# Kernel tuning notes

Measured on AMD Instinct MI355X. Metric: run time of the kernel, lower is better.

The kernel has to match this reference:

```python
import jax, jax.numpy as jnp
import numpy as np

S, B, D, A = 8192, 64, 512, 256


def setup_inputs() -> dict:
    key = jax.random.key(0)
    ks = jax.random.split(key, 7)
    return {
        "x": jax.random.normal(ks[0], (S, B, D), dtype=jnp.float32),
        "h": jax.random.normal(ks[1], (1, B, D), dtype=jnp.float32),
        "Wx": jax.random.normal(ks[2], (A, D), dtype=jnp.float32) * (1.0 / np.sqrt(D)),
        "bx": jax.random.normal(ks[3], (A,), dtype=jnp.float32) * 0.01,
        "Wh": jax.random.normal(ks[4], (A, D), dtype=jnp.float32) * (1.0 / np.sqrt(D)),
        "Wt": jax.random.normal(ks[5], (1, A), dtype=jnp.float32) * (1.0 / np.sqrt(A)),
        "bt": jax.random.normal(ks[6], (1,), dtype=jnp.float32) * 0.01,
    }


def reference(x, h, Wx, bx, Wh, Wt, bt):
    # x: (S, B, D) seq-first; h: (1, B, D) hidden state.
    # All Conv1d ops have kernel size 1 -> plain per-position matmuls.
    xb = jnp.transpose(x, (1, 0, 2))               # (B, S, D)
    wx = jnp.einsum('bsd,ad->bas', xb, Wx) + bx[None, :, None]   # (B, A, S)
    h0 = h.transpose(1, 0, 2).reshape(-1, h.shape[-1])           # (B, D)
    wh = h0 @ Wh.T                                                # (B, A)
    # score conv (A -> 1) on tanh(wx + wh), then softmax over seq dim
    score = jnp.einsum('a,bas->bs', Wt[0], jnp.tanh(wx + wh[:, :, None])) + bt[0]  # (B, S)
    attn = jax.nn.softmax(score, axis=-1)                         # (B, S)
    out = jnp.einsum('bs,bsd->bd', attn, xb)                      # (B, D)
    return out
```

## Files before the change

### kernel.cpp

```cpp
#include <hip/hip_runtime.h>


#define S_DIM 8192
#define B_DIM 64
#define D_DIM 512
#define A_DIM 256
#define BM 32
#define NTILES 256

typedef _Float16 half8 __attribute__((ext_vector_type(8)));
typedef float f32x4 __attribute__((ext_vector_type(4)));

__device__ __forceinline__ float tanh_fast(float x) {
  float e = __expf(2.0f * x);
  return 1.0f - 2.0f * __builtin_amdgcn_rcpf(e + 1.0f);
}

__global__ void __launch_bounds__(256)
convw_kernel(const float* __restrict__ Wx, _Float16* __restrict__ Wp) {
  const int idx = (blockIdx.x * 256 + threadIdx.x) * 8;
  const int a = idx >> 9;
  const int k = idx & 511;
  f32x4 va = *(const f32x4*)(Wx + idx);
  f32x4 vb = *(const f32x4*)(Wx + idx + 4);
  half8 hx;
#pragma unroll
  for (int i = 0; i < 4; ++i) { hx[i] = (_Float16)va[i]; hx[4 + i] = (_Float16)vb[i]; }
  const int ta = a >> 4, fr = a & 15;
  const int tk = k >> 5, fg = (k >> 3) & 3;
  *(half8*)(Wp + (ta * 16 + tk) * 512 + (fg * 16 + fr) * 8) = hx;
}

__global__ void __launch_bounds__(256)
whb_kernel(const float* __restrict__ h, const float* __restrict__ Wh,
           const float* __restrict__ bx, float* __restrict__ whb) {
  __shared__ float hs[D_DIM];
  const int b = blockIdx.x, tid = threadIdx.x;
  hs[tid] = h[b * D_DIM + tid];
  hs[tid + 256] = h[b * D_DIM + 256 + tid];
  __syncthreads();
  const int g = tid >> 4, i = tid & 15;
  for (int pass = 0; pass < 16; ++pass) {
    const int a = pass * 16 + g;
    const f32x4* wrow = (const f32x4*)(Wh + (size_t)a * D_DIM);
    float dot = 0.f;
#pragma unroll
    for (int k = 0; k < 8; ++k) {
      f32x4 wv = wrow[i + k * 16];
      f32x4 hv = *(const f32x4*)(hs + (i + k * 16) * 4);
      dot += wv[0] * hv[0] + wv[1] * hv[1] + wv[2] * hv[2] + wv[3] * hv[3];
    }
#pragma unroll
    for (int mask = 1; mask < 16; mask <<= 1) dot += __shfl_xor(dot, mask, 64);
    if (i == 0) whb[b * A_DIM + a] = dot + bx[a];
  }
}

__global__ void __launch_bounds__(256, 4)
paa_main(const float* __restrict__ x, const _Float16* __restrict__ Wp,
         const float* __restrict__ whb, const float* __restrict__ Wt,
         float* __restrict__ m_arr, float* __restrict__ l_arr,
         float* __restrict__ acc_arr) {
  __shared__ _Float16 xs[BM * D_DIM];
  __shared__ float scorep[4 * BM];

  const int tid = threadIdx.x;
  const int lane = tid & 63;
  const int wv = tid >> 6;
  const int b = blockIdx.x;
  const int tile = blockIdx.y;

  const int fr = lane & 15, fg = lane >> 4;
  const int akey = fr & 7;
  const _Float16* wp = Wp + wv * (4 * 16 * 512) + lane * 8;

  float wt_a[4], whb_a[4];
#pragma unroll
  for (int nf = 0; nf < 4; ++nf) {
    wt_a[nf]  = Wt[wv * 64 + nf * 16 + fr];
    whb_a[nf] = whb[b * A_DIM + wv * 64 + nf * 16 + fr];
  }

  const int srow = tid >> 3, sseg = tid & 7;
  const int skey = srow & 7;
  {
    const float* rp = x + ((size_t)(tile * BM + srow) * B_DIM + b) * D_DIM;
    f32x4 sa[4], sb[4];
#pragma unroll
    for (int p = 0; p < 4; ++p) {
      sa[p] = *(const f32x4*)(rp + p * 64 + sseg * 8);
      sb[p] = *(const f32x4*)(rp + p * 64 + sseg * 8 + 4);
    }
#pragma unroll
    for (int p = 0; p < 4; ++p) {
      half8 hx;
#pragma unroll
      for (int j = 0; j < 4; ++j) { hx[j] = (_Float16)sa[p][j]; hx[4 + j] = (_Float16)sb[p][j]; }
      const int ch = p * 8 + sseg;
      *(half8*)(xs + srow * D_DIM + ((ch ^ skey) * 8)) = hx;
    }
#pragma unroll
    for (int p = 0; p < 4; ++p) {
      sa[p] = *(const f32x4*)(rp + (4 + p) * 64 + sseg * 8);
      sb[p] = *(const f32x4*)(rp + (4 + p) * 64 + sseg * 8 + 4);
    }
#pragma unroll
    for (int p = 0; p < 4; ++p) {
      half8 hx;
#pragma unroll
      for (int j = 0; j < 4; ++j) { hx[j] = (_Float16)sa[p][j]; hx[4 + j] = (_Float16)sb[p][j]; }
      const int ch = (4 + p) * 8 + sseg;
      *(half8*)(xs + srow * D_DIM + ((ch ^ skey) * 8)) = hx;
    }
  }
  __syncthreads();

  f32x4 acc[2][4];
#pragma unroll
  for (int mi = 0; mi < 2; ++mi)
#pragma unroll
    for (int nf = 0; nf < 4; ++nf) acc[mi][nf] = (f32x4){0.f, 0.f, 0.f, 0.f};
#pragma unroll
  for (int tk = 0; tk < 16; ++tk) {
    const int slot = ((tk * 4 + fg) ^ akey) * 8;
    half8 af0 = *(const half8*)(xs + (fr) * D_DIM + slot);
    half8 af1 = *(const half8*)(xs + (16 + fr) * D_DIM + slot);
    half8 bf0 = *(const half8*)(wp + (0 * 16 + tk) * 512);
    half8 bf1 = *(const half8*)(wp + (1 * 16 + tk) * 512);
    half8 bf2 = *(const half8*)(wp + (2 * 16 + tk) * 512);
    half8 bf3 = *(const half8*)(wp + (3 * 16 + tk) * 512);
    acc[0][0] = __builtin_amdgcn_mfma_f32_16x16x32_f16(af0, bf0, acc[0][0], 0, 0, 0);
    acc[0][1] = __builtin_amdgcn_mfma_f32_16x16x32_f16(af0, bf1, acc[0][1], 0, 0, 0);
    acc[0][2] = __builtin_amdgcn_mfma_f32_16x16x32_f16(af0, bf2, acc[0][2], 0, 0, 0);
    acc[0][3] = __builtin_amdgcn_mfma_f32_16x16x32_f16(af0, bf3, acc[0][3], 0, 0, 0);
    acc[1][0] = __builtin_amdgcn_mfma_f32_16x16x32_f16(af1, bf0, acc[1][0], 0, 0, 0);
    acc[1][1] = __builtin_amdgcn_mfma_f32_16x16x32_f16(af1, bf1, acc[1][1], 0, 0, 0);
    acc[1][2] = __builtin_amdgcn_mfma_f32_16x16x32_f16(af1, bf2, acc[1][2], 0, 0, 0);
    acc[1][3] = __builtin_amdgcn_mfma_f32_16x16x32_f16(af1, bf3, acc[1][3], 0, 0, 0);
  }

  {
    float part[2][4];
#pragma unroll
    for (int mi = 0; mi < 2; ++mi)
#pragma unroll
      for (int r = 0; r < 4; ++r) part[mi][r] = 0.f;
#pragma unroll
    for (int nf = 0; nf < 4; ++nf)
#pragma unroll
      for (int mi = 0; mi < 2; ++mi)
#pragma unroll
        for (int r = 0; r < 4; ++r)
          part[mi][r] += wt_a[nf] * tanh_fast(acc[mi][nf][r] + whb_a[nf]);
#pragma unroll
    for (int mask = 1; mask < 16; mask <<= 1)
#pragma unroll
      for (int mi = 0; mi < 2; ++mi)
#pragma unroll
        for (int r = 0; r < 4; ++r) part[mi][r] += __shfl_xor(part[mi][r], mask, 64);
    if (fr == 0) {
#pragma unroll
      for (int mi = 0; mi < 2; ++mi)
#pragma unroll
        for (int r = 0; r < 4; ++r)
          scorep[wv * BM + mi * 16 + fg * 4 + r] = part[mi][r];
    }
  }
  __syncthreads();

  const int rl = lane & 31;
  float sv = scorep[rl] + scorep[BM + rl] + scorep[2 * BM + rl] + scorep[3 * BM + rl];
  float m = sv;
#pragma unroll
  for (int mask = 1; mask < 32; mask <<= 1) m = fmaxf(m, __shfl_xor(m, mask, 64));
  float p = __expf(sv - m);
  float lsum = p;
#pragma unroll
  for (int mask = 1; mask < 32; mask <<= 1) lsum += __shfl_xor(lsum, mask, 64);
  if (tid == 0) {
    m_arr[b * NTILES + tile] = m;
    l_arr[b * NTILES + tile] = lsum;
  }

  {
    const int q = lane >> 4;
    const int ch = wv * 16 + (lane & 15);
    float wacc[8];
#pragma unroll
    for (int j = 0; j < 8; ++j) wacc[j] = 0.f;
#pragma unroll
    for (int k = 0; k < 8; ++k) {
      const int row = q * 8 + k;
      const float pr = __shfl(p, row, 64);
      half8 xv = *(const half8*)(xs + row * D_DIM + ((ch ^ (row & 7)) * 8));
#pragma unroll
      for (int j = 0; j < 8; ++j) wacc[j] += pr * (float)xv[j];
    }
#pragma unroll
    for (int j = 0; j < 8; ++j) wacc[j] += __shfl_xor(wacc[j], 16, 64);
#pragma unroll
    for (int j = 0; j < 8; ++j) wacc[j] += __shfl_xor(wacc[j], 32, 64);
    if (lane < 16) {
      float* ob = acc_arr + ((size_t)(b * NTILES + tile)) * D_DIM + ch * 8;
      *(f32x4*)(ob) = (f32x4){wacc[0], wacc[1], wacc[2], wacc[3]};
      *(f32x4*)(ob + 4) = (f32x4){wacc[4], wacc[5], wacc[6], wacc[7]};
    }
  }
}

__global__ void __launch_bounds__(512)
combine_kernel(const float* __restrict__ m_arr, const float* __restrict__ l_arr,
               const float* __restrict__ acc_arr, float* __restrict__ out) {
  __shared__ float ml[NTILES], ls[NTILES], wl[NTILES];
  const int b = blockIdx.x, tid = threadIdx.x;
  if (tid < NTILES) {
    ml[tid] = m_arr[b * NTILES + tid];
    ls[tid] = l_arr[b * NTILES + tid];
  }
  __syncthreads();
  float M = -1e30f;
  for (int i = 0; i < NTILES; ++i) M = fmaxf(M, ml[i]);
  if (tid < NTILES) wl[tid] = __expf(ml[tid] - M);
  __syncthreads();
  float L = 0.f;
  for (int i = 0; i < NTILES; ++i) L += wl[i] * ls[i];
  float sum = 0.f;
  const size_t base = (size_t)b * NTILES * D_DIM + tid;
  for (int i = 0; i < NTILES; ++i) sum += wl[i] * acc_arr[base + (size_t)i * D_DIM];
  out[b * D_DIM + tid] = sum / L;
}

extern "C" void kernel_launch(void* const* d_in, const int* in_sizes, int n_in,
                              void* d_out, int out_size, void* d_ws, size_t ws_size,
                              hipStream_t stream) {
  const float* x = (const float*)d_in[0];
  const float* h = (const float*)d_in[1];
  const float* Wx = (const float*)d_in[2];
  const float* bx = (const float*)d_in[3];
  const float* Wh = (const float*)d_in[4];
  const float* Wt = (const float*)d_in[5];

  char* ws = (char*)d_ws;
  _Float16* Wp = (_Float16*)ws;
  float* whb = (float*)(ws + 262144);
  float* m_arr = (float*)(ws + 262144 + 65536);
  float* l_arr = (float*)(ws + 262144 + 65536 + 65536);
  float* acc_arr = (float*)(ws + 262144 + 3 * 65536);

  hipLaunchKernelGGL(convw_kernel, dim3(64), dim3(256), 0, stream, Wx, Wp);
  hipLaunchKernelGGL(whb_kernel, dim3(B_DIM), dim3(256), 0, stream, h, Wh, bx, whb);
  hipLaunchKernelGGL(paa_main, dim3(B_DIM, NTILES), dim3(256), 0, stream,
                     x, Wp, whb, Wt, m_arr, l_arr, acc_arr);
  hipLaunchKernelGGL(combine_kernel, dim3(B_DIM), dim3(512), 0, stream,
                     m_arr, l_arr, acc_arr, (float*)d_out);
}
```

Baseline: 368.0 us.

## Double attention tile to 64 rows with 512-thread blocks and 8 waves

Each block now handles 64 sequence rows using 512 threads, so there are 8 waves. Each wave covers 32 attention channels across 4 row fragments, where before each wave covered 64 channels across 2 fragments. This halves the number of tiles, the partial softmax outputs and the combine work, and each wave now loads half as much Wp per tile. The trade-off is doubled LDS (64 KB per block), which lowers occupancy. Each wave also does more fp16 x loads from LDS, and the reductions gain an extra shuffle.

Result: slower. 416.4 us (+13.1%).

```diff
diff --git a/kernel.cpp b/kernel.cpp
--- a/kernel.cpp
+++ b/kernel.cpp
@@ -5,8 +5,8 @@
 #define B_DIM 64
 #define D_DIM 512
 #define A_DIM 256
-#define BM 32
-#define NTILES 256
+#define BM 64
+#define NTILES 128
 
 typedef _Float16 half8 __attribute__((ext_vector_type(8)));
 typedef float f32x4 __attribute__((ext_vector_type(4)));
@@ -56,13 +56,13 @@
   }
 }
 
-__global__ void __launch_bounds__(256, 4)
+__global__ void __launch_bounds__(512, 4)
 paa_main(const float* __restrict__ x, const _Float16* __restrict__ Wp,
          const float* __restrict__ whb, const float* __restrict__ Wt,
          float* __restrict__ m_arr, float* __restrict__ l_arr,
          float* __restrict__ acc_arr) {
   __shared__ _Float16 xs[BM * D_DIM];
-  __shared__ float scorep[4 * BM];
+  __shared__ float scorep[8 * BM];
 
   const int tid = threadIdx.x;
   const int lane = tid & 63;
@@ -72,13 +72,13 @@
 
   const int fr = lane & 15, fg = lane >> 4;
   const int akey = fr & 7;
-  const _Float16* wp = Wp + wv * (4 * 16 * 512) + lane * 8;
-
-  float wt_a[4], whb_a[4];
-#pragma unroll
-  for (int nf = 0; nf < 4; ++nf) {
-    wt_a[nf]  = Wt[wv * 64 + nf * 16 + fr];
-    whb_a[nf] = whb[b * A_DIM + wv * 64 + nf * 16 + fr];
+  const _Float16* wp = Wp + (wv * 2) * (16 * 512) + lane * 8;
+
+  float wt_a[2], whb_a[2];
+#pragma unroll
+  for (int nf = 0; nf < 2; ++nf) {
+    wt_a[nf]  = Wt[wv * 32 + nf * 16 + fr];
+    whb_a[nf] = whb[b * A_DIM + wv * 32 + nf * 16 + fr];
   }
 
   const int srow = tid >> 3, sseg = tid & 7;
@@ -115,76 +115,77 @@
   }
   __syncthreads();
 
-  f32x4 acc[2][4];
-#pragma unroll
-  for (int mi = 0; mi < 2; ++mi)
-#pragma unroll
-    for (int nf = 0; nf < 4; ++nf) acc[mi][nf] = (f32x4){0.f, 0.f, 0.f, 0.f};
+  f32x4 acc[4][2];
+#pragma unroll
+  for (int mf = 0; mf < 4; ++mf)
+#pragma unroll
+    for (int nf = 0; nf < 2; ++nf) acc[mf][nf] = (f32x4){0.f, 0.f, 0.f, 0.f};
 #pragma unroll
   for (int tk = 0; tk < 16; ++tk) {
     const int slot = ((tk * 4 + fg) ^ akey) * 8;
     half8 af0 = *(const half8*)(xs + (fr) * D_DIM + slot);
     half8 af1 = *(const half8*)(xs + (16 + fr) * D_DIM + slot);
+    half8 af2 = *(const half8*)(xs + (32 + fr) * D_DIM + slot);
+    half8 af3 = *(const half8*)(xs + (48 + fr) * D_DIM + slot);
     half8 bf0 = *(const half8*)(wp + (0 * 16 + tk) * 512);
     half8 bf1 = *(const half8*)(wp + (1 * 16 + tk) * 512);
-    half8 bf2 = *(const half8*)(wp + (2 * 16 + tk) * 512);
-    half8 bf3 = *(const half8*)(wp + (3 * 16 + tk) * 512);
     acc[0][0] = __builtin_amdgcn_mfma_f32_16x16x32_f16(af0, bf0, acc[0][0], 0, 0, 0);
     acc[0][1] = __builtin_amdgcn_mfma_f32_16x16x32_f16(af0, bf1, acc[0][1], 0, 0, 0);
-    acc[0][2] = __builtin_amdgcn_mfma_f32_16x16x32_f16(af0, bf2, acc[0][2], 0, 0, 0);
-    acc[0][3] = __builtin_amdgcn_mfma_f32_16x16x32_f16(af0, bf3, acc[0][3], 0, 0, 0);
     acc[1][0] = __builtin_amdgcn_mfma_f32_16x16x32_f16(af1, bf0, acc[1][0], 0, 0, 0);
     acc[1][1] = __builtin_amdgcn_mfma_f32_16x16x32_f16(af1, bf1, acc[1][1], 0, 0, 0);
-    acc[1][2] = __builtin_amdgcn_mfma_f32_16x16x32_f16(af1, bf2, acc[1][2], 0, 0, 0);
-    acc[1][3] = __builtin_amdgcn_mfma_f32_16x16x32_f16(af1, bf3, acc[1][3], 0, 0, 0);
+    acc[2][0] = __builtin_amdgcn_mfma_f32_16x16x32_f16(af2, bf0, acc[2][0], 0, 0, 0);
+    acc[2][1] = __builtin_amdgcn_mfma_f32_16x16x32_f16(af2, bf1, acc[2][1], 0, 0, 0);
+    acc[3][0] = __builtin_amdgcn_mfma_f32_16x16x32_f16(af3, bf0, acc[3][0], 0, 0, 0);
+    acc[3][1] = __builtin_amdgcn_mfma_f32_16x16x32_f16(af3, bf1, acc[3][1], 0, 0, 0);
   }
 
   {
-    float part[2][4];
-#pragma unroll
-    for (int mi = 0; mi < 2; ++mi)
-#pragma unroll
-      for (int r = 0; r < 4; ++r) part[mi][r] = 0.f;
-#pragma unroll
-    for (int nf = 0; nf < 4; ++nf)
-#pragma unroll
-      for (int mi = 0; mi < 2; ++mi)
+    float part[4][4];
+#pragma unroll
+    for (int mf = 0; mf < 4; ++mf)
+#pragma unroll
+      for (int r = 0; r < 4; ++r) part[mf][r] = 0.f;
+#pragma unroll
+    for (int nf = 0; nf < 2; ++nf)
+#pragma unroll
+      for (int mf = 0; mf < 4; ++mf)
 #pragma unroll
         for (int r = 0; r < 4; ++r)
-          part[mi][r] += wt_a[nf] * tanh_fast(acc[mi][nf][r] + whb_a[nf]);
+          part[mf][r] += wt_a[nf] * tanh_fast(acc[mf][nf][r] + whb_a[nf]);
 #pragma unroll
     for (int mask = 1; mask < 16; mask <<= 1)
 #pragma unroll
-      for (int mi = 0; mi < 2; ++mi)
-#pragma unroll
-        for (int r = 0; r < 4; ++r) part[mi][r] += __shfl_xor(part[mi][r], mask, 64);
+      for (int mf = 0; mf < 4; ++mf)
+#pragma unroll
+        for (int r = 0; r < 4; ++r) part[mf][r] += __shfl_xor(part[mf][r], mask, 64);
     if (fr == 0) {
 #pragma unroll
-      for (int mi = 0; mi < 2; ++mi)
+      for (int mf = 0; mf < 4; ++mf)
 #pragma unroll
         for (int r = 0; r < 4; ++r)
-          scorep[wv * BM + mi * 16 + fg * 4 + r] = part[mi][r];
-    }
-  }
-  __syncthreads();
-
-  const int rl = lane & 31;
-  float sv = scorep[rl] + scorep[BM + rl] + scorep[2 * BM + rl] + scorep[3 * BM + rl];
+          scorep[wv * BM + mf * 16 + fg * 4 + r] = part[mf][r];
+    }
+  }
+  __syncthreads();
+
+  float sv = 0.f;
+#pragma unroll
+  for (int w = 0; w < 8; ++w) sv += scorep[w * BM + lane];
   float m = sv;
 #pragma unroll
-  for (int mask = 1; mask < 32; mask <<= 1) m = fmaxf(m, __shfl_xor(m, mask, 64));
+  for (int mask = 1; mask < 64; mask <<= 1) m = fmaxf(m, __shfl_xor(m, mask, 64));
   float p = __expf(sv - m);
   float lsum = p;
 #pragma unroll
-  for (int mask = 1; mask < 32; mask <<= 1) lsum += __shfl_xor(lsum, mask, 64);
+  for (int mask = 1; mask < 64; mask <<= 1) lsum += __shfl_xor(lsum, mask, 64);
   if (tid == 0) {
     m_arr[b * NTILES + tile] = m;
     l_arr[b * NTILES + tile] = lsum;
   }
 
   {
-    const int q = lane >> 4;
-    const int ch = wv * 16 + (lane & 15);
+    const int q = lane >> 3;
+    const int ch = wv * 8 + (lane & 7);
     float wacc[8];
 #pragma unroll
     for (int j = 0; j < 8; ++j) wacc[j] = 0.f;
@@ -197,10 +198,12 @@
       for (int j = 0; j < 8; ++j) wacc[j] += pr * (float)xv[j];
     }
 #pragma unroll
+    for (int j = 0; j < 8; ++j) wacc[j] += __shfl_xor(wacc[j], 8, 64);
+#pragma unroll
     for (int j = 0; j < 8; ++j) wacc[j] += __shfl_xor(wacc[j], 16, 64);
 #pragma unroll
     for (int j = 0; j < 8; ++j) wacc[j] += __shfl_xor(wacc[j], 32, 64);
-    if (lane < 16) {
+    if (lane < 8) {
       float* ob = acc_arr + ((size_t)(b * NTILES + tile)) * D_DIM + ch * 8;
       *(f32x4*)(ob) = (f32x4){wacc[0], wacc[1], wacc[2], wacc[3]};
       *(f32x4*)(ob + 4) = (f32x4){wacc[4], wacc[5], wacc[6], wacc[7]};
@@ -249,7 +252,7 @@
 
   hipLaunchKernelGGL(convw_kernel, dim3(64), dim3(256), 0, stream, Wx, Wp);
   hipLaunchKernelGGL(whb_kernel, dim3(B_DIM), dim3(256), 0, stream, h, Wh, bx, whb);
-  hipLaunchKernelGGL(paa_main, dim3(B_DIM, NTILES), dim3(256), 0, stream,
+  hipLaunchKernelGGL(paa_main, dim3(B_DIM, NTILES), dim3(512), 0, stream,
                      x, Wp, whb, Wt, m_arr, l_arr, acc_arr);
   hipLaunchKernelGGL(combine_kernel, dim3(B_DIM), dim3(512), 0, stream,
                      m_arr, l_arr, acc_arr, (float*)d_out);
```

## Process eight tiles per block with register prefetch of next x tile

Applied to the files above, without the earlier changes.

Turns the one-tile-per-block grid into a persistent-style loop where each block handles eight consecutive 32-row tiles for one batch element. The first half of the next tile is loaded into registers during the tanh/softmax phase, and the second half is loaded after the barrier and converted into shared memory. The goal is to overlap global loads of x with compute and to amortize block launch and weight-setup cost. In exchange there are fewer blocks (2048), extra barriers per tile, and more register pressure from the prefetch buffers.

Result: slower. 1.284 ms (+249.0%).

```diff
diff --git a/kernel.cpp b/kernel.cpp
--- a/kernel.cpp
+++ b/kernel.cpp
@@ -7,9 +7,16 @@
 #define A_DIM 256
 #define BM 32
 #define NTILES 256
+#define TPB 8
+#define NBLK 2048
 
 typedef _Float16 half8 __attribute__((ext_vector_type(8)));
 typedef float f32x4 __attribute__((ext_vector_type(4)));
+
+#define BAR() do { __builtin_amdgcn_sched_barrier(0); \
+  asm volatile("s_waitcnt lgkmcnt(0)" ::: "memory"); \
+  __builtin_amdgcn_s_barrier(); \
+  __builtin_amdgcn_sched_barrier(0); } while (0)
 
 __device__ __forceinline__ float tanh_fast(float x) {
   float e = __expf(2.0f * x);
@@ -67,8 +74,9 @@
   const int tid = threadIdx.x;
   const int lane = tid & 63;
   const int wv = tid >> 6;
-  const int b = blockIdx.x;
-  const int tile = blockIdx.y;
+  const int b = blockIdx.x & 63;
+  const int sgrp = blockIdx.x >> 6;
+  const int t0 = sgrp * TPB;
 
   const int fr = lane & 15, fg = lane >> 4;
   const int akey = fr & 7;
@@ -83,8 +91,9 @@
 
   const int srow = tid >> 3, sseg = tid & 7;
   const int skey = srow & 7;
+
   {
-    const float* rp = x + ((size_t)(tile * BM + srow) * B_DIM + b) * D_DIM;
+    const float* rp = x + ((size_t)(t0 * BM + srow) * B_DIM + b) * D_DIM;
     f32x4 sa[4], sb[4];
 #pragma unroll
     for (int p = 0; p < 4; ++p) {
@@ -96,8 +105,7 @@
       half8 hx;
 #pragma unroll
       for (int j = 0; j < 4; ++j) { hx[j] = (_Float16)sa[p][j]; hx[4 + j] = (_Float16)sb[p][j]; }
-      const int ch = p * 8 + sseg;
-      *(half8*)(xs + srow * D_DIM + ((ch ^ skey) * 8)) = hx;
+      *(half8*)(xs + srow * D_DIM + (((p * 8 + sseg) ^ skey) * 8)) = hx;
     }
 #pragma unroll
     for (int p = 0; p < 4; ++p) {
@@ -109,102 +117,144 @@
       half8 hx;
 #pragma unroll
       for (int j = 0; j < 4; ++j) { hx[j] = (_Float16)sa[p][j]; hx[4 + j] = (_Float16)sb[p][j]; }
-      const int ch = (4 + p) * 8 + sseg;
-      *(half8*)(xs + srow * D_DIM + ((ch ^ skey) * 8)) = hx;
+      *(half8*)(xs + srow * D_DIM + ((((4 + p) * 8 + sseg) ^ skey) * 8)) = hx;
     }
   }
   __syncthreads();
 
-  f32x4 acc[2][4];
-#pragma unroll
-  for (int mi = 0; mi < 2; ++mi)
-#pragma unroll
-    for (int nf = 0; nf < 4; ++nf) acc[mi][nf] = (f32x4){0.f, 0.f, 0.f, 0.f};
-#pragma unroll
-  for (int tk = 0; tk < 16; ++tk) {
-    const int slot = ((tk * 4 + fg) ^ akey) * 8;
-    half8 af0 = *(const half8*)(xs + (fr) * D_DIM + slot);
-    half8 af1 = *(const half8*)(xs + (16 + fr) * D_DIM + slot);
-    half8 bf0 = *(const half8*)(wp + (0 * 16 + tk) * 512);
-    half8 bf1 = *(const half8*)(wp + (1 * 16 + tk) * 512);
-    half8 bf2 = *(const half8*)(wp + (2 * 16 + tk) * 512);
-    half8 bf3 = *(const half8*)(wp + (3 * 16 + tk) * 512);
-    acc[0][0] = __builtin_amdgcn_mfma_f32_16x16x32_f16(af0, bf0, acc[0][0], 0, 0, 0);
-    acc[0][1] = __builtin_amdgcn_mfma_f32_16x16x32_f16(af0, bf1, acc[0][1], 0, 0, 0);
-    acc[0][2] = __builtin_amdgcn_mfma_f32_16x16x32_f16(af0, bf2, acc[0][2], 0, 0, 0);
-    acc[0][3] = __builtin_amdgcn_mfma_f32_16x16x32_f16(af0, bf3, acc[0][3], 0, 0, 0);
-    acc[1][0] = __builtin_amdgcn_mfma_f32_16x16x32_f16(af1, bf0, acc[1][0], 0, 0, 0);
-    acc[1][1] = __builtin_amdgcn_mfma_f32_16x16x32_f16(af1, bf1, acc[1][1], 0, 0, 0);
-    acc[1][2] = __builtin_amdgcn_mfma_f32_16x16x32_f16(af1, bf2, acc[1][2], 0, 0, 0);
-    acc[1][3] = __builtin_amdgcn_mfma_f32_16x16x32_f16(af1, bf3, acc[1][3], 0, 0, 0);
-  }
-
-  {
-    float part[2][4];
+  for (int i = 0; i < TPB; ++i) {
+    const int tile = t0 + i;
+    const bool pf = (i + 1 < TPB);
+    const float* rpn = x + ((size_t)((tile + 1) * BM + srow) * B_DIM + b) * D_DIM;
+
+    f32x4 acc[2][4];
 #pragma unroll
     for (int mi = 0; mi < 2; ++mi)
 #pragma unroll
-      for (int r = 0; r < 4; ++r) part[mi][r] = 0.f;
-#pragma unroll
-    for (int nf = 0; nf < 4; ++nf)
+      for (int nf = 0; nf < 4; ++nf) acc[mi][nf] = (f32x4){0.f, 0.f, 0.f, 0.f};
+#pragma unroll
+    for (int tk = 0; tk < 16; ++tk) {
+      const int slot = ((tk * 4 + fg) ^ akey) * 8;
+      half8 af0 = *(const half8*)(xs + (fr) * D_DIM + slot);
+      half8 af1 = *(const half8*)(xs + (16 + fr) * D_DIM + slot);
+      half8 bf0 = *(const half8*)(wp + (0 * 16 + tk) * 512);
+      half8 bf1 = *(const half8*)(wp + (1 * 16 + tk) * 512);
+      half8 bf2 = *(const half8*)(wp + (2 * 16 + tk) * 512);
+      half8 bf3 = *(const half8*)(wp + (3 * 16 + tk) * 512);
+      acc[0][0] = __builtin_amdgcn_mfma_f32_16x16x32_f16(af0, bf0, acc[0][0], 0, 0, 0);
+      acc[0][1] = __builtin_amdgcn_mfma_f32_16x16x32_f16(af0, bf1, acc[0][1], 0, 0, 0);
+      acc[0][2] = __builtin_amdgcn_mfma_f32_16x16x32_f16(af0, bf2, acc[0][2], 0, 0, 0);
+      acc[0][3] = __builtin_amdgcn_mfma_f32_16x16x32_f16(af0, bf3, acc[0][3], 0, 0, 0);
+      acc[1][0] = __builtin_amdgcn_mfma_f32_16x16x32_f16(af1, bf0, acc[1][0], 0, 0, 0);
+      acc[1][1] = __builtin_amdgcn_mfma_f32_16x16x32_f16(af1, bf1, acc[1][1], 0, 0, 0);
+      acc[1][2] = __builtin_amdgcn_mfma_f32_16x16x32_f16(af1, bf2, acc[1][2], 0, 0, 0);
+      acc[1][3] = __builtin_amdgcn_mfma_f32_16x16x32_f16(af1, bf3, acc[1][3], 0, 0, 0);
+    }
+
+    f32x4 pa[4], pb[4];
+    if (pf) {
+#pragma unroll
+      for (int p = 0; p < 4; ++p) {
+        pa[p] = *(const f32x4*)(rpn + p * 64 + sseg * 8);
+        pb[p] = *(const f32x4*)(rpn + p * 64 + sseg * 8 + 4);
+      }
+    }
+    __builtin_amdgcn_sched_barrier(0);
+
+    {
+      float part[2][4];
 #pragma unroll
       for (int mi = 0; mi < 2; ++mi)
 #pragma unroll
-        for (int r = 0; r < 4; ++r)
-          part[mi][r] += wt_a[nf] * tanh_fast(acc[mi][nf][r] + whb_a[nf]);
-#pragma unroll
-    for (int mask = 1; mask < 16; mask <<= 1)
-#pragma unroll
-      for (int mi = 0; mi < 2; ++mi)
-#pragma unroll
-        for (int r = 0; r < 4; ++r) part[mi][r] += __shfl_xor(part[mi][r], mask, 64);
-    if (fr == 0) {
-#pragma unroll
-      for (int mi = 0; mi < 2; ++mi)
-#pragma unroll
-        for (int r = 0; r < 4; ++r)
-          scorep[wv * BM + mi * 16 + fg * 4 + r] = part[mi][r];
-    }
-  }
-  __syncthreads();
-
-  const int rl = lane & 31;
-  float sv = scorep[rl] + scorep[BM + rl] + scorep[2 * BM + rl] + scorep[3 * BM + rl];
-  float m = sv;
-#pragma unroll
-  for (int mask = 1; mask < 32; mask <<= 1) m = fmaxf(m, __shfl_xor(m, mask, 64));
-  float p = __expf(sv - m);
-  float lsum = p;
-#pragma unroll
-  for (int mask = 1; mask < 32; mask <<= 1) lsum += __shfl_xor(lsum, mask, 64);
-  if (tid == 0) {
-    m_arr[b * NTILES + tile] = m;
-    l_arr[b * NTILES + tile] = lsum;
-  }
-
-  {
-    const int q = lane >> 4;
-    const int ch = wv * 16 + (lane & 15);
-    float wacc[8];
-#pragma unroll
-    for (int j = 0; j < 8; ++j) wacc[j] = 0.f;
-#pragma unroll
-    for (int k = 0; k < 8; ++k) {
-      const int row = q * 8 + k;
-      const float pr = __shfl(p, row, 64);
-      half8 xv = *(const half8*)(xs + row * D_DIM + ((ch ^ (row & 7)) * 8));
-#pragma unroll
-      for (int j = 0; j < 8; ++j) wacc[j] += pr * (float)xv[j];
-    }
-#pragma unroll
-    for (int j = 0; j < 8; ++j) wacc[j] += __shfl_xor(wacc[j], 16, 64);
-#pragma unroll
-    for (int j = 0; j < 8; ++j) wacc[j] += __shfl_xor(wacc[j], 32, 64);
-    if (lane < 16) {
-      float* ob = acc_arr + ((size_t)(b * NTILES + tile)) * D_DIM + ch * 8;
-      *(f32x4*)(ob) = (f32x4){wacc[0], wacc[1], wacc[2], wacc[3]};
-      *(f32x4*)(ob + 4) = (f32x4){wacc[4], wacc[5], wacc[6], wacc[7]};
-    }
+        for (int r = 0; r < 4; ++r) part[mi][r] = 0.f;
+#pragma unroll
+      for (int nf = 0; nf < 4; ++nf)
+#pragma unroll
+        for (int mi = 0; mi < 2; ++mi)
+#pragma unroll
+          for (int r = 0; r < 4; ++r)
+            part[mi][r] += wt_a[nf] * tanh_fast(acc[mi][nf][r] + whb_a[nf]);
+#pragma unroll
+      for (int mask = 1; mask < 16; mask <<= 1)
+#pragma unroll
+        for (int mi = 0; mi < 2; ++mi)
+#pragma unroll
+          for (int r = 0; r < 4; ++r) part[mi][r] += __shfl_xor(part[mi][r], mask, 64);
+      if (fr == 0) {
+#pragma unroll
+        for (int mi = 0; mi < 2; ++mi)
+#pragma unroll
+          for (int r = 0; r < 4; ++r)
+            scorep[wv * BM + mi * 16 + fg * 4 + r] = part[mi][r];
+      }
+    }
+
+    BAR();
+
+    const int rl = lane & 31;
+    float sv = scorep[rl] + scorep[BM + rl] + scorep[2 * BM + rl] + scorep[3 * BM + rl];
+    float m = sv;
+#pragma unroll
+    for (int mask = 1; mask < 32; mask <<= 1) m = fmaxf(m, __shfl_xor(m, mask, 64));
+    float p = __expf(sv - m);
+    float lsum = p;
+#pragma unroll
+    for (int mask = 1; mask < 32; mask <<= 1) lsum += __shfl_xor(lsum, mask, 64);
+    if (tid == 0) {
+      m_arr[b * NTILES + tile] = m;
+      l_arr[b * NTILES + tile] = lsum;
+    }
+
+    {
+      const int q = lane >> 4;
+      const int ch = wv * 16 + (lane & 15);
+      float wacc[8];
+#pragma unroll
+      for (int j = 0; j < 8; ++j) wacc[j] = 0.f;
+#pragma unroll
+      for (int k = 0; k < 8; ++k) {
+        const int row = q * 8 + k;
+        const float pr = __shfl(p, row, 64);
+        half8 xv = *(const half8*)(xs + row * D_DIM + ((ch ^ (row & 7)) * 8));
+#pragma unroll
+        for (int j = 0; j < 8; ++j) wacc[j] += pr * (float)xv[j];
+      }
+#pragma unroll
+      for (int j = 0; j < 8; ++j) wacc[j] += __shfl_xor(wacc[j], 16, 64);
+#pragma unroll
+      for (int j = 0; j < 8; ++j) wacc[j] += __shfl_xor(wacc[j], 32, 64);
+      if (lane < 16) {
+        float* ob = acc_arr + ((size_t)(b * NTILES + tile)) * D_DIM + ch * 8;
+        *(f32x4*)(ob) = (f32x4){wacc[0], wacc[1], wacc[2], wacc[3]};
+        *(f32x4*)(ob + 4) = (f32x4){wacc[4], wacc[5], wacc[6], wacc[7]};
+      }
+    }
+
+    BAR();
+
+    if (pf) {
+#pragma unroll
+      for (int p = 0; p < 4; ++p) {
+        half8 hx;
+#pragma unroll
+        for (int j = 0; j < 4; ++j) { hx[j] = (_Float16)pa[p][j]; hx[4 + j] = (_Float16)pb[p][j]; }
+        *(half8*)(xs + srow * D_DIM + (((p * 8 + sseg) ^ skey) * 8)) = hx;
+      }
+#pragma unroll
+      for (int p = 0; p < 4; ++p) {
+        pa[p] = *(const f32x4*)(rpn + (4 + p) * 64 + sseg * 8);
+        pb[p] = *(const f32x4*)(rpn + (4 + p) * 64 + sseg * 8 + 4);
+      }
+#pragma unroll
+      for (int p = 0; p < 4; ++p) {
+        half8 hx;
+#pragma unroll
+        for (int j = 0; j < 4; ++j) { hx[j] = (_Float16)pa[p][j]; hx[4 + j] = (_Float16)pb[p][j]; }
+        *(half8*)(xs + srow * D_DIM + ((((4 + p) * 8 + sseg) ^ skey) * 8)) = hx;
+      }
+    }
+
+    __syncthreads();
   }
 }
 
@@ -249,7 +299,7 @@
 
   hipLaunchKernelGGL(convw_kernel, dim3(64), dim3(256), 0, stream, Wx, Wp);
   hipLaunchKernelGGL(whb_kernel, dim3(B_DIM), dim3(256), 0, stream, h, Wh, bx, whb);
-  hipLaunchKernelGGL(paa_main, dim3(B_DIM, NTILES), dim3(256), 0, stream,
+  hipLaunchKernelGGL(paa_main, dim3(NBLK), dim3(256), 0, stream,
                      x, Wp, whb, Wt, m_arr, l_arr, acc_arr);
   hipLaunchKernelGGL(combine_kernel, dim3(B_DIM), dim3(512), 0, stream,
                      m_arr, l_arr, acc_arr, (float*)d_out);
```
